# Kernel tuning notes

Hardware: AMD Instinct MI355X
Metric: run time of the kernel (lower is better)

## Reference

```python
import jax, jax.numpy as jnp
import numpy as np

B, N, M = 2, 256, 512
IN_F, OUT_F = 256, 128
NEG_INF = -1.0e12


def setup_inputs() -> dict:
    key = jax.random.key(0)
    kx, ka, kw, kv = jax.random.split(key, 4)
    X = jax.random.normal(kx, (B, N, IN_F), dtype=jnp.float32)
    # node-edge incidence (0/1), kept float as in the torch module
    A = jax.random.randint(ka, (B, N, M), 0, 2).astype(jnp.float32)
    # xavier-uniform-ish scale: gain*sqrt(6/(fan_in+fan_out))
    w_scale = 1.414 * np.sqrt(6.0 / (IN_F + OUT_F))
    a_scale = 1.414 * np.sqrt(6.0 / (2 * OUT_F + 1))
    W = jax.random.uniform(kw, (IN_F, OUT_F), jnp.float32, -w_scale, w_scale)
    a = jax.random.uniform(kv, (2 * OUT_F, 1), jnp.float32, -a_scale, a_scale)
    return {"X": X, "A": A, "W": W, "a": a}


def reference(X, A, W, a):
    H = X @ W                                   # [B, N, F]
    F_ = H.shape[-1]
    # per-edge degree, zeros clamped to 1
    degree = jnp.sum(A, axis=1)[..., None]      # [B, M, 1]
    degree = jnp.where(degree == 0, 1.0, degree)
    Em = jnp.einsum('bnm,bnf->bmf', A, H) / degree   # [B, M, F]
    # faithful replication of torch: cat along dim=1 then view (note: NOT a
    # per-pair concat along features; rows of H and Em get interleaved)
    Hrep = jnp.tile(H, (1, 1, M)).reshape(B, N * M, F_)   # [B, N*M, F]
    EmRep = jnp.tile(Em, (1, N, 1))                        # [B, N*M, F]
    a_input = jnp.concatenate([Hrep, EmRep], axis=1).reshape(B, N, M, 2 * F_)
    e = jax.nn.leaky_relu(jnp.squeeze(a_input @ a, -1), negative_slope=0.01)  # [B, N, M]
    attention = jax.nn.softmax(jnp.where(A > 0, e, NEG_INF), axis=2)          # [B, N, M]
    h_prime = jnp.einsum('bnm,bnf->bmf', attention, H)                         # [B, M, F]
    return h_prime
```

## Files before the change

### kernel.cpp

```cpp
#include <hip/hip_runtime.h>

#define NN 256
#define MM 512
#define INF_ 256
#define OUTF 128

__global__ __launch_bounds__(256) void k_gemm(const float* __restrict__ X,
                                              const float* __restrict__ W,
                                              const float* __restrict__ avec,
                                              float* __restrict__ H,
                                              float* __restrict__ h0,
                                              float* __restrict__ h1,
                                              float* __restrict__ cH,
                                              float* __restrict__ S) {
    const int blk = blockIdx.x;
    const int t = threadIdx.x;
    const int bn0 = blk * 2;
    __shared__ float xs[2][INF_];
    __shared__ float4 sacc[2][8][32];
    xs[0][t] = X[bn0 * INF_ + t];
    xs[1][t] = X[(bn0 + 1) * INF_ + t];
    __syncthreads();

    const int f4 = t & 31, kg = t >> 5;
    const float4* W4 = (const float4*)W;
    float4 acc0 = {0.f, 0.f, 0.f, 0.f}, acc1 = {0.f, 0.f, 0.f, 0.f};
    const int k0 = kg * 32;
#pragma unroll 8
    for (int i = 0; i < 32; ++i) {
        const int k = k0 + i;
        float4 w = W4[k * 32 + f4];
        float x0v = xs[0][k], x1v = xs[1][k];
        acc0.x = fmaf(x0v, w.x, acc0.x); acc0.y = fmaf(x0v, w.y, acc0.y);
        acc0.z = fmaf(x0v, w.z, acc0.z); acc0.w = fmaf(x0v, w.w, acc0.w);
        acc1.x = fmaf(x1v, w.x, acc1.x); acc1.y = fmaf(x1v, w.y, acc1.y);
        acc1.z = fmaf(x1v, w.z, acc1.z); acc1.w = fmaf(x1v, w.w, acc1.w);
    }
    sacc[0][kg][f4] = acc0;
    sacc[1][kg][f4] = acc1;
    __syncthreads();

    if (t < 64) {
        const int r = t >> 5, fb = t & 31;
        float4 s = {0.f, 0.f, 0.f, 0.f};
#pragma unroll
        for (int j = 0; j < 8; ++j) {
            float4 v = sacc[r][j][fb];
            s.x += v.x; s.y += v.y; s.z += v.z; s.w += v.w;
        }
        ((float4*)H)[(bn0 + r) * 32 + fb] = s;
        const float4* av4 = (const float4*)avec;
        float4 a0 = av4[fb], a1 = av4[32 + fb];
        float p0 = s.x*a0.x + s.y*a0.y + s.z*a0.z + s.w*a0.w;
        float p1 = s.x*a1.x + s.y*a1.y + s.z*a1.z + s.w*a1.w;
#pragma unroll
        for (int off = 16; off >= 1; off >>= 1) {
            p0 += __shfl_xor(p0, off);
            p1 += __shfl_xor(p1, off);
        }
        if ((t & 31) == 0) {
            const int bn = bn0 + r;
            h0[bn] = p0;
            h1[bn] = p1;
            float hA = p0 + p1;
            cH[bn] = hA > 0.f ? hA : 0.01f * hA;
            const int n = bn & 255;
            if (n >= 128) S[(bn >> 8) * 128 + n - 128] = 0.f;
        }
    }
}

__global__ __launch_bounds__(256) void k_emg(const float* __restrict__ A,
                                             const float* __restrict__ h0,
                                             const float* __restrict__ h1,
                                             const float* __restrict__ cH,
                                             float* __restrict__ g,
                                             float* __restrict__ rs0,
                                             float* __restrict__ rs1,
                                             float* __restrict__ S) {
    const int blk = blockIdx.x;
    const int t = threadIdx.x;
    if (blk < 32) {
        const int b = blk >> 4, mq = blk & 15;
        const int m_l = t & 31, n_l = t >> 5;
        __shared__ float sh0[NN], sh1[NN];
        __shared__ float sd[256], ss0[256], ss1[256];
        __shared__ float se0[32], se1[32], sg[16];
        sh0[t] = h0[b * NN + t];
        sh1[t] = h1[b * NN + t];
        __syncthreads();
        const float* Ap = A + (size_t)b * NN * MM + mq * 32 + m_l;
        float d = 0.f, s0 = 0.f, s1 = 0.f;
#pragma unroll 8
        for (int i = 0; i < 32; ++i) {
            int n = n_l * 32 + i;
            float av = Ap[n * MM];
            d += av;
            s0 += av * sh0[n];
            s1 += av * sh1[n];
        }
        sd[t] = d; ss0[t] = s0; ss1[t] = s1;
        __syncthreads();
        if (t < 32) {
            float D = 0.f, S0 = 0.f, S1 = 0.f;
#pragma unroll
            for (int j = 0; j < 8; ++j) {
                D  += sd[j * 32 + t];
                S0 += ss0[j * 32 + t];
                S1 += ss1[j * 32 + t];
            }
            if (D == 0.f) D = 1.f;
            se0[t] = S0 / D;
            se1[t] = S1 / D;
        }
        __syncthreads();
        if (t < 16) {
            float v = se0[2 * t] + se1[2 * t + 1];
            v = v > 0.f ? v : 0.01f * v;
            float gv = expf(v);
            g[b * MM + 16 * mq + t] = gv;
            g[b * MM + 256 + 16 * mq + t] = gv;
            sg[t] = gv;
        }
        __syncthreads();
        {
            const int u = t & 15, ng = t >> 4;
            const float gv = sg[u];
            const float* Alo = A + (size_t)b * NN * MM + 16 * mq + u;
#pragma unroll
            for (int step = 0; step < 8; ++step) {
                int n = 128 + ng + 16 * step;
                const float* Ar = Alo + (size_t)n * MM;
                float val = gv * (Ar[0] + Ar[256]);
                val += __shfl_xor(val, 1);
                val += __shfl_xor(val, 2);
                val += __shfl_xor(val, 4);
                val += __shfl_xor(val, 8);
                if (u == 0) atomicAdd(&S[b * 128 + n - 128], val);
            }
        }
    } else {
        const int wv = t >> 6, lane = t & 63;
        const int l = (blk - 32) * 4 + wv;
        const int b = l >> 7, n = l & 127;
        const int bn = b * NN + n;
        const float* Ar = A + (size_t)bn * MM;
        float c0 = 0.f, c1 = 0.f;
#pragma unroll
        for (int i = 0; i < 8; ++i) {
            float av = Ar[lane + 64 * i];
            if (i < 4) c0 += av; else c1 += av;
        }
#pragma unroll
        for (int off = 32; off >= 1; off >>= 1) {
            c0 += __shfl_xor(c0, off);
            c1 += __shfl_xor(c1, off);
        }
        if (lane == 0) {
            float ch0 = cH[b * NN + 2 * n];
            float ch1 = cH[b * NN + 2 * n + 1];
            float mx = fmaxf(c0 > 0.f ? ch0 : -INFINITY,
                             c1 > 0.f ? ch1 : -INFINITY);
            float e0 = c0 > 0.f ? expf(ch0 - mx) : 0.f;
            float e1 = c1 > 0.f ? expf(ch1 - mx) : 0.f;
            float inv = 1.f / (c0 * e0 + c1 * e1);
            rs0[bn] = e0 * inv;
            rs1[bn] = e1 * inv;
        }
    }
}

__global__ __launch_bounds__(256) void k_out(const float* __restrict__ A,
                                             const float* __restrict__ H,
                                             const float* __restrict__ g,
                                             const float* __restrict__ rs0,
                                             const float* __restrict__ rs1,
                                             const float* __restrict__ S,
                                             float* __restrict__ out) {
    __shared__ float sW[NN];
    __shared__ float sA[4][NN];
    __shared__ float4 sacc[8][4][32];
    const int blk = blockIdx.x;
    const int b = blk >> 7, mq = blk & 127;
    const int m_base = 4 * mq;
    const int t = threadIdx.x;
    if (t < 128) {
        sW[t] = ((mq < 64) ? rs0 : rs1)[b * NN + t];
    } else {
        sW[t] = 1.f / S[b * 128 + (t - 128)];
    }
    {
        const float4* Ar = (const float4*)(A + (size_t)(b * NN + t) * MM + m_base);
        float4 a = Ar[0];
        sA[0][t] = a.x; sA[1][t] = a.y; sA[2][t] = a.z; sA[3][t] = a.w;
    }
    __syncthreads();
    const int f4 = t & 31, ng = t >> 5;
    const float4* H4 = (const float4*)H + (size_t)b * NN * 32 + f4;
    float4 A0 = {0.f,0.f,0.f,0.f}, A1 = {0.f,0.f,0.f,0.f};
    float4 A2 = {0.f,0.f,0.f,0.f}, A3 = {0.f,0.f,0.f,0.f};
    const int n0 = ng * 32;
#pragma unroll 8
    for (int i = 0; i < 32; ++i) {
        const int n = n0 + i;
        float w = sW[n];
        float4 hv = H4[n * 32];
        float c0 = sA[0][n] * w;
        float c1 = sA[1][n] * w;
        float c2 = sA[2][n] * w;
        float c3 = sA[3][n] * w;
        A0.x = fmaf(c0, hv.x, A0.x); A0.y = fmaf(c0, hv.y, A0.y);
        A0.z = fmaf(c0, hv.z, A0.z); A0.w = fmaf(c0, hv.w, A0.w);
        A1.x = fmaf(c1, hv.x, A1.x); A1.y = fmaf(c1, hv.y, A1.y);
        A1.z = fmaf(c1, hv.z, A1.z); A1.w = fmaf(c1, hv.w, A1.w);
        A2.x = fmaf(c2, hv.x, A2.x); A2.y = fmaf(c2, hv.y, A2.y);
        A2.z = fmaf(c2, hv.z, A2.z); A2.w = fmaf(c2, hv.w, A2.w);
        A3.x = fmaf(c3, hv.x, A3.x); A3.y = fmaf(c3, hv.y, A3.y);
        A3.z = fmaf(c3, hv.z, A3.z); A3.w = fmaf(c3, hv.w, A3.w);
    }
    sacc[ng][0][f4] = A0;
    sacc[ng][1][f4] = A1;
    sacc[ng][2][f4] = A2;
    sacc[ng][3][f4] = A3;
    __syncthreads();
    if (t < 128) {
        const int ml = t >> 5, fb = t & 31;
        float4 lo = {0.f,0.f,0.f,0.f}, hi = {0.f,0.f,0.f,0.f};
#pragma unroll
        for (int j = 0; j < 4; ++j) {
            float4 vl = sacc[j][ml][fb];
            float4 vh = sacc[4 + j][ml][fb];
            lo.x += vl.x; lo.y += vl.y; lo.z += vl.z; lo.w += vl.w;
            hi.x += vh.x; hi.y += vh.y; hi.z += vh.z; hi.w += vh.w;
        }
        const int m = m_base + ml;
        const float eE = g[b * MM + m];
        float4 r;
        r.x = lo.x + eE * hi.x;
        r.y = lo.y + eE * hi.y;
        r.z = lo.z + eE * hi.z;
        r.w = lo.w + eE * hi.w;
        ((float4*)out)[((size_t)b * MM + m) * 32 + fb] = r;
    }
}

extern "C" void kernel_launch(void* const* d_in, const int* in_sizes, int n_in,
                              void* d_out, int out_size, void* d_ws, size_t ws_size,
                              hipStream_t stream) {
    const float* X = (const float*)d_in[0];
    const float* A = (const float*)d_in[1];
    const float* W = (const float*)d_in[2];
    const float* a = (const float*)d_in[3];
    float* out = (float*)d_out;
    float* ws = (float*)d_ws;

    float* H   = ws;
    float* h0  = ws + 65536;
    float* h1  = ws + 66048;
    float* cH  = ws + 66560;
    float* g   = ws + 67072;
    float* rs0 = ws + 68096;
    float* rs1 = ws + 68608;
    float* S   = ws + 69120;

    k_gemm<<<256, 256, 0, stream>>>(X, W, a, H, h0, h1, cH, S);
    k_emg<<<96, 256, 0, stream>>>(A, h0, h1, cH, g, rs0, rs1, S);
    k_out<<<256, 256, 0, stream>>>(A, H, g, rs0, rs1, S, out);
}
```

Before: 23.89 us.

## Fuse row softmax weights into GEMM kernel and widen edge-aggregation grid

The per-row incidence counts and the two-way softmax weights (rs0/rs1) are now computed inside the GEMM kernel. Otherwise-idle threads read a row of A there, and the leaky-relu scores stay in shared memory instead of a global cH buffer. The edge-mean kernel no longer carries the row-softmax branch. Its edge work is split over 64 blocks of 16 edges each instead of 32 blocks of 32, to spread the heavy A-column reduction across more CUs. This adds global A reads to the GEMM kernel and more atomics into S.

Measured after the change: 21.25 us. 1.12x faster.

```diff
diff --git a/kernel.cpp b/kernel.cpp
--- a/kernel.cpp
+++ b/kernel.cpp
@@ -6,18 +6,23 @@
 #define OUTF 128
 
 __global__ __launch_bounds__(256) void k_gemm(const float* __restrict__ X,
+                                              const float* __restrict__ A,
                                               const float* __restrict__ W,
                                               const float* __restrict__ avec,
                                               float* __restrict__ H,
                                               float* __restrict__ h0,
                                               float* __restrict__ h1,
-                                              float* __restrict__ cH,
+                                              float* __restrict__ rs0,
+                                              float* __restrict__ rs1,
                                               float* __restrict__ S) {
     const int blk = blockIdx.x;
     const int t = threadIdx.x;
+    const int b = blk >> 7, q = blk & 127;
     const int bn0 = blk * 2;
     __shared__ float xs[2][INF_];
     __shared__ float4 sacc[2][8][32];
+    __shared__ float sch[2];
+    __shared__ float scnt[2];
     xs[0][t] = X[bn0 * INF_ + t];
     xs[1][t] = X[(bn0 + 1) * INF_ + t];
     __syncthreads();
@@ -63,109 +68,101 @@
             h0[bn] = p0;
             h1[bn] = p1;
             float hA = p0 + p1;
-            cH[bn] = hA > 0.f ? hA : 0.01f * hA;
-            const int n = bn & 255;
-            if (n >= 128) S[(bn >> 8) * 128 + n - 128] = 0.f;
-        }
+            sch[r] = hA > 0.f ? hA : 0.01f * hA;
+        }
+    } else if (t < 128) {
+        const int l = t - 64;
+        const float* Ar = A + (size_t)(b * NN + q) * MM;
+        float c0 = 0.f, c1 = 0.f;
+#pragma unroll
+        for (int i = 0; i < 8; ++i) {
+            float av = Ar[l + 64 * i];
+            if (i < 4) c0 += av; else c1 += av;
+        }
+#pragma unroll
+        for (int off = 32; off >= 1; off >>= 1) {
+            c0 += __shfl_xor(c0, off);
+            c1 += __shfl_xor(c1, off);
+        }
+        if (l == 0) { scnt[0] = c0; scnt[1] = c1; }
+    }
+    __syncthreads();
+    if (t == 0) {
+        const float c0 = scnt[0], c1 = scnt[1];
+        const float ch0 = sch[0], ch1 = sch[1];
+        float mx = fmaxf(c0 > 0.f ? ch0 : -INFINITY,
+                         c1 > 0.f ? ch1 : -INFINITY);
+        float e0 = c0 > 0.f ? expf(ch0 - mx) : 0.f;
+        float e1 = c1 > 0.f ? expf(ch1 - mx) : 0.f;
+        float inv = 1.f / (c0 * e0 + c1 * e1);
+        rs0[b * NN + q] = e0 * inv;
+        rs1[b * NN + q] = e1 * inv;
+        S[b * 128 + q] = 0.f;
     }
 }
 
 __global__ __launch_bounds__(256) void k_emg(const float* __restrict__ A,
                                              const float* __restrict__ h0,
                                              const float* __restrict__ h1,
-                                             const float* __restrict__ cH,
                                              float* __restrict__ g,
-                                             float* __restrict__ rs0,
-                                             float* __restrict__ rs1,
                                              float* __restrict__ S) {
     const int blk = blockIdx.x;
     const int t = threadIdx.x;
-    if (blk < 32) {
-        const int b = blk >> 4, mq = blk & 15;
-        const int m_l = t & 31, n_l = t >> 5;
-        __shared__ float sh0[NN], sh1[NN];
-        __shared__ float sd[256], ss0[256], ss1[256];
-        __shared__ float se0[32], se1[32], sg[16];
-        sh0[t] = h0[b * NN + t];
-        sh1[t] = h1[b * NN + t];
-        __syncthreads();
-        const float* Ap = A + (size_t)b * NN * MM + mq * 32 + m_l;
-        float d = 0.f, s0 = 0.f, s1 = 0.f;
+    const int b = blk >> 5, mq = blk & 31;
+    const int m_l = t & 15, n_l = t >> 4;
+    __shared__ float sh0[NN], sh1[NN];
+    __shared__ float sd[256], ss0[256], ss1[256];
+    __shared__ float se0[16], se1[16], sg[8];
+    sh0[t] = h0[b * NN + t];
+    sh1[t] = h1[b * NN + t];
+    __syncthreads();
+    const float* Ap = A + (size_t)b * NN * MM + mq * 16 + m_l;
+    float d = 0.f, s0 = 0.f, s1 = 0.f;
 #pragma unroll 8
-        for (int i = 0; i < 32; ++i) {
-            int n = n_l * 32 + i;
-            float av = Ap[n * MM];
-            d += av;
-            s0 += av * sh0[n];
-            s1 += av * sh1[n];
-        }
-        sd[t] = d; ss0[t] = s0; ss1[t] = s1;
-        __syncthreads();
-        if (t < 32) {
-            float D = 0.f, S0 = 0.f, S1 = 0.f;
-#pragma unroll
-            for (int j = 0; j < 8; ++j) {
-                D  += sd[j * 32 + t];
-                S0 += ss0[j * 32 + t];
-                S1 += ss1[j * 32 + t];
-            }
-            if (D == 0.f) D = 1.f;
-            se0[t] = S0 / D;
-            se1[t] = S1 / D;
-        }
-        __syncthreads();
-        if (t < 16) {
-            float v = se0[2 * t] + se1[2 * t + 1];
-            v = v > 0.f ? v : 0.01f * v;
-            float gv = expf(v);
-            g[b * MM + 16 * mq + t] = gv;
-            g[b * MM + 256 + 16 * mq + t] = gv;
-            sg[t] = gv;
-        }
-        __syncthreads();
-        {
-            const int u = t & 15, ng = t >> 4;
-            const float gv = sg[u];
-            const float* Alo = A + (size_t)b * NN * MM + 16 * mq + u;
-#pragma unroll
-            for (int step = 0; step < 8; ++step) {
-                int n = 128 + ng + 16 * step;
-                const float* Ar = Alo + (size_t)n * MM;
-                float val = gv * (Ar[0] + Ar[256]);
-                val += __shfl_xor(val, 1);
-                val += __shfl_xor(val, 2);
-                val += __shfl_xor(val, 4);
-                val += __shfl_xor(val, 8);
-                if (u == 0) atomicAdd(&S[b * 128 + n - 128], val);
-            }
-        }
-    } else {
-        const int wv = t >> 6, lane = t & 63;
-        const int l = (blk - 32) * 4 + wv;
-        const int b = l >> 7, n = l & 127;
-        const int bn = b * NN + n;
-        const float* Ar = A + (size_t)bn * MM;
-        float c0 = 0.f, c1 = 0.f;
-#pragma unroll
-        for (int i = 0; i < 8; ++i) {
-            float av = Ar[lane + 64 * i];
-            if (i < 4) c0 += av; else c1 += av;
-        }
-#pragma unroll
-        for (int off = 32; off >= 1; off >>= 1) {
-            c0 += __shfl_xor(c0, off);
-            c1 += __shfl_xor(c1, off);
-        }
-        if (lane == 0) {
-            float ch0 = cH[b * NN + 2 * n];
-            float ch1 = cH[b * NN + 2 * n + 1];
-            float mx = fmaxf(c0 > 0.f ? ch0 : -INFINITY,
-                             c1 > 0.f ? ch1 : -INFINITY);
-            float e0 = c0 > 0.f ? expf(ch0 - mx) : 0.f;
-            float e1 = c1 > 0.f ? expf(ch1 - mx) : 0.f;
-            float inv = 1.f / (c0 * e0 + c1 * e1);
-            rs0[bn] = e0 * inv;
-            rs1[bn] = e1 * inv;
+    for (int i = 0; i < 16; ++i) {
+        int n = n_l * 16 + i;
+        float av = Ap[n * MM];
+        d += av;
+        s0 += av * sh0[n];
+        s1 += av * sh1[n];
+    }
+    sd[t] = d; ss0[t] = s0; ss1[t] = s1;
+    __syncthreads();
+    if (t < 16) {
+        float D = 0.f, S0 = 0.f, S1 = 0.f;
+#pragma unroll
+        for (int j = 0; j < 16; ++j) {
+            D  += sd[j * 16 + t];
+            S0 += ss0[j * 16 + t];
+            S1 += ss1[j * 16 + t];
+        }
+        if (D == 0.f) D = 1.f;
+        se0[t] = S0 / D;
+        se1[t] = S1 / D;
+    }
+    __syncthreads();
+    if (t < 8) {
+        float v = se0[2 * t] + se1[2 * t + 1];
+        v = v > 0.f ? v : 0.01f * v;
+        float gv = expf(v);
+        g[b * MM + 8 * mq + t] = gv;
+        g[b * MM + 256 + 8 * mq + t] = gv;
+        sg[t] = gv;
+    }
+    __syncthreads();
+    {
+        const int u = t & 7, ng = t >> 3;
+        const float gv = sg[u];
+        const float* Alo = A + (size_t)b * NN * MM + 8 * mq + u;
+#pragma unroll
+        for (int step = 0; step < 4; ++step) {
+            int n = 128 + ng + 32 * step;
+            const float* Ar = Alo + (size_t)n * MM;
+            float val = gv * (Ar[0] + Ar[256]);
+            val += __shfl_xor(val, 1);
+            val += __shfl_xor(val, 2);
+            val += __shfl_xor(val, 4);
+            if (u == 0) atomicAdd(&S[b * 128 + n - 128], val);
         }
     }
 }
@@ -257,13 +254,12 @@
     float* H   = ws;
     float* h0  = ws + 65536;
     float* h1  = ws + 66048;
-    float* cH  = ws + 66560;
-    float* g   = ws + 67072;
-    float* rs0 = ws + 68096;
-    float* rs1 = ws + 68608;
-    float* S   = ws + 69120;
-
-    k_gemm<<<256, 256, 0, stream>>>(X, W, a, H, h0, h1, cH, S);
-    k_emg<<<96, 256, 0, stream>>>(A, h0, h1, cH, g, rs0, rs1, S);
+    float* g   = ws + 66560;
+    float* rs0 = ws + 67584;
+    float* rs1 = ws + 68096;
+    float* S   = ws + 68608;
+
+    k_gemm<<<256, 256, 0, stream>>>(X, A, W, a, H, h0, h1, rs0, rs1, S);
+    k_emg<<<64, 256, 0, stream>>>(A, h0, h1, g, S);
     k_out<<<256, 256, 0, stream>>>(A, H, g, rs0, rs1, S, out);
 }
```
